# Optimization experiments

Measured on AMD Instinct MI355X. Metric: run time of the kernel, lower is better.

The kernel has to match this reference:

```python
import jax, jax.numpy as jnp
import numpy as np

USR_NUM = 100000
D_IN = 32
D_HID = 32
D_MID = 16
D_OUT = 2
N_EDGES = 1600000
EPS = 1e-16  # matches torch_geometric.utils.softmax denominator eps


def _glorot(key, shape):
    fan_in, fan_out = shape[0], shape[1]
    lim = np.sqrt(6.0 / (fan_in + fan_out))
    return jax.random.uniform(key, shape, jnp.float32, -lim, lim)


def setup_inputs() -> dict:
    key = jax.random.key(0)
    ks = jax.random.split(key, 16)
    inp = {
        "edge_index": jax.random.randint(ks[0], (2, N_EDGES), 0, USR_NUM, dtype=jnp.int64)
        if jax.config.jax_enable_x64 else jax.random.randint(ks[0], (2, N_EDGES), 0, USR_NUM).astype(jnp.int32),
        "emb": jax.random.normal(ks[1], (USR_NUM, D_IN), jnp.float32),
        # conv1: TransformerConv(32 -> 32, heads=1)
        "Wq1": _glorot(ks[2], (D_IN, D_HID)), "bq1": jnp.zeros((D_HID,), jnp.float32),
        "Wk1": _glorot(ks[3], (D_IN, D_HID)), "bk1": jnp.zeros((D_HID,), jnp.float32),
        "Wv1": _glorot(ks[4], (D_IN, D_HID)), "bv1": jnp.zeros((D_HID,), jnp.float32),
        "Ws1": _glorot(ks[5], (D_IN, D_HID)), "bs1": jnp.zeros((D_HID,), jnp.float32),
        # conv2: TransformerConv(32 -> 16, heads=1)
        "Wq2": _glorot(ks[6], (D_HID, D_MID)), "bq2": jnp.zeros((D_MID,), jnp.float32),
        "Wk2": _glorot(ks[7], (D_HID, D_MID)), "bk2": jnp.zeros((D_MID,), jnp.float32),
        "Wv2": _glorot(ks[8], (D_HID, D_MID)), "bv2": jnp.zeros((D_MID,), jnp.float32),
        "Ws2": _glorot(ks[9], (D_HID, D_MID)), "bs2": jnp.zeros((D_MID,), jnp.float32),
        # output: Linear(16 -> 2)
        "Wo": _glorot(ks[10], (D_MID, D_OUT)), "bo": jnp.zeros((D_OUT,), jnp.float32),
    }
    return inp


def transformer_conv(x, src, dst, Wq, bq, Wk, bk, Wv, bv, Ws, bs, n_nodes):
    # edge (j=src -> i=dst): alpha_ij = softmax_i( <q_i, k_j> / sqrt(d) )
    d = Wq.shape[1]
    q = (x @ Wq + bq)[dst]          # [E, d]
    k = (x @ Wk + bk)[src]          # [E, d]
    v = (x @ Wv + bv)[src]          # [E, d]
    alpha = jnp.sum(q * k, axis=-1) / jnp.sqrt(jnp.float32(d))  # [E]
    # segment softmax over incoming edges of each destination node
    seg_max = jax.ops.segment_max(alpha, dst, num_segments=n_nodes)  # [N]
    e = jnp.exp(alpha - seg_max[dst])
    seg_sum = jax.ops.segment_sum(e, dst, num_segments=n_nodes)      # [N]
    w = e / (seg_sum[dst] + EPS)
    agg = jax.ops.segment_sum(v * w[:, None], dst, num_segments=n_nodes)  # [N, d]
    return agg + x @ Ws + bs  # root/skip connection (PyG default root_weight=True)


def reference(edge_index, emb,
              Wq1, bq1, Wk1, bk1, Wv1, bv1, Ws1, bs1,
              Wq2, bq2, Wk2, bk2, Wv2, bv2, Ws2, bs2,
              Wo, bo):
    src, dst = edge_index[0], edge_index[1]
    h = transformer_conv(emb, src, dst, Wq1, bq1, Wk1, bk1, Wv1, bv1, Ws1, bs1, USR_NUM)
    h = jax.nn.relu(h)
    h = transformer_conv(h, src, dst, Wq2, bq2, Wk2, bk2, Wv2, bv2, Ws2, bs2, USR_NUM)
    h = jax.nn.relu(h)
    return h @ Wo + bo  # [N, 2]
```

## Files before the change

kernel.cpp:

```cpp
#include <hip/hip_runtime.h>
#include <hip/hip_bf16.h>

typedef __hip_bfloat16 bf16;
typedef unsigned int uint;
typedef unsigned short ushort;

#define N_NODES 100000
#define N_EDGES_C 1600000
#define NSB 196
#define NSBP 200
#define SBCAP 10240
#define RND 2048
#define EPB (RND / 256)
#define NBIN 64
#define G_RAD ((N_EDGES_C + RND - 1) / RND)
#define NSLOT (NSB * 512)

__device__ __forceinline__ float ldf(const void* p, long i, int isbf) {
    return isbf ? __bfloat162float(((const bf16*)p)[i]) : ((const float*)p)[i];
}
__device__ __forceinline__ int ldidx(const int* ei, long pos, int is64) {
    return is64 ? ei[2 * pos] : ei[pos];
}
__device__ __forceinline__ ushort bfb(float x) {
    bf16 h = __float2bfloat16(x);
    return *(ushort*)&h;
}
__device__ __forceinline__ float bl(uint u) { return __uint_as_float(u << 16); }
__device__ __forceinline__ float bh(uint u) { return __uint_as_float(u & 0xFFFF0000u); }

__global__ void setup_kernel(
    const void* emb, const int* ei,
    const void* Wq1, const void* bq1, const void* Wk1, const void* bk1,
    const void* Wv1, const void* bv1, const void* Ws1, const void* bs1,
    const void* Wq2, const void* bq2, const void* Wk2, const void* bk2,
    const void* Wv2, const void* bv2, const void* Ws2, const void* bs2,
    const void* Wo, const void* bo,
    int* flags, float* wp1, float* bp1, float* wp2, float* bp2, float* woF,
    int* curSB) {
    __shared__ int sf0;
    int t = threadIdx.x;
    if (t < 64) {
        const bf16* pb = (const bf16*)emb;
        int bad = 0;
        for (int i = t; i < 256; i += 64) {
            float v = __bfloat162float(pb[i]);
            if (!(v > -1.0e6f && v < 1.0e6f)) bad++;
        }
        int nz = 0;
        for (int i = 2 * t + 1; i < 256; i += 128) nz += (ei[i] != 0) ? 1 : 0;
#pragma unroll
        for (int m = 32; m >= 1; m >>= 1) {
            bad += __shfl_xor(bad, m, 64);
            nz  += __shfl_xor(nz, m, 64);
        }
        if (t == 0) {
            int f0 = (bad <= 8) ? 1 : 0;
            flags[0] = f0;
            flags[1] = (nz == 0) ? 1 : 0;
            sf0 = f0;
        }
    }
    __syncthreads();
    int isbf = sf0;
    for (int i = t; i < 1024; i += 256) {
        wp1[i]        = ldf(Wq1, i, isbf);
        wp1[1024 + i] = ldf(Wk1, i, isbf);
        wp1[2048 + i] = ldf(Wv1, i, isbf);
        wp1[3072 + i] = ldf(Ws1, i, isbf);
    }
    for (int i = t; i < 512; i += 256) {
        wp2[i]        = ldf(Wq2, i, isbf);
        wp2[512 + i]  = ldf(Wk2, i, isbf);
        wp2[1024 + i] = ldf(Wv2, i, isbf);
        wp2[1536 + i] = ldf(Ws2, i, isbf);
    }
    if (t < 32) {
        bp1[t] = ldf(bq1, t, isbf); bp1[32 + t] = ldf(bk1, t, isbf);
        bp1[64 + t] = ldf(bv1, t, isbf); bp1[96 + t] = ldf(bs1, t, isbf);
        woF[t] = ldf(Wo, t, isbf);
    }
    if (t < 16) {
        bp2[t] = ldf(bq2, t, isbf); bp2[16 + t] = ldf(bk2, t, isbf);
        bp2[32 + t] = ldf(bv2, t, isbf); bp2[48 + t] = ldf(bs2, t, isbf);
    }
    if (t < 2) woF[32 + t] = ldf(bo, t, isbf);
    curSB[t] = 0;
}

template <int DOUT, bool RUNTIME_DTYPE>
__device__ __forceinline__ void node_linear_body(
    const void* __restrict__ X, const float* __restrict__ wpack,
    const float* __restrict__ bpack, const int* __restrict__ flags,
    float* __restrict__ q, ushort* __restrict__ kvb, float* __restrict__ s,
    int bid, float* __restrict__ sW, float* __restrict__ sbias, float* __restrict__ sX) {
    const int TPN = DOUT / 4;
    const int NPB = 256 / TPN;
    const int W_ELEMS = 4 * 32 * DOUT;

    const float4* wp4 = (const float4*)wpack;
    float4* sW4 = (float4*)sW;
    for (int i = threadIdx.x; i < W_ELEMS / 4; i += 256) sW4[i] = wp4[i];
    if (threadIdx.x < 4 * DOUT) sbias[threadIdx.x] = bpack[threadIdx.x];
    const int base = bid * NPB * 32;
    bool useBf = RUNTIME_DTYPE && (flags[0] != 0);
    if (useBf) {
        for (int i = threadIdx.x; i < NPB * 32; i += 256) {
            int g = base + i;
            float xv = (g < N_NODES * 32) ? __bfloat162float(((const bf16*)X)[g]) : 0.0f;
            sX[(i >> 5) * 36 + (i & 31)] = xv;
        }
    } else {
        for (int i = threadIdx.x; i < NPB * 32; i += 256) {
            int g = base + i;
            sX[(i >> 5) * 36 + (i & 31)] = (g < N_NODES * 32) ? ((const float*)X)[g] : 0.0f;
        }
    }
    __syncthreads();

    int l = threadIdx.x / TPN;
    int c4 = (threadIdx.x % TPN) * 4;
    int n = bid * NPB + l;
    if (n >= N_NODES) return;

    float xr[32];
#pragma unroll
    for (int j = 0; j < 8; j++) {
        float4 t4 = *(const float4*)&sX[l * 36 + 4 * j];
        xr[4 * j] = t4.x; xr[4 * j + 1] = t4.y; xr[4 * j + 2] = t4.z; xr[4 * j + 3] = t4.w;
    }
    float acc[4][4];
#pragma unroll
    for (int m = 0; m < 4; m++)
#pragma unroll
        for (int j = 0; j < 4; j++) acc[m][j] = sbias[m * DOUT + c4 + j];

#pragma unroll
    for (int t = 0; t < 32; t++) {
#pragma unroll
        for (int m = 0; m < 4; m++) {
            float4 w = *(const float4*)&sW[(m * 32 + t) * DOUT + c4];
            acc[m][0] += xr[t] * w.x;
            acc[m][1] += xr[t] * w.y;
            acc[m][2] += xr[t] * w.z;
            acc[m][3] += xr[t] * w.w;
        }
    }
    size_t o = (size_t)n * DOUT + c4;
    *(float4*)&q[o] = make_float4(acc[0][0], acc[0][1], acc[0][2], acc[0][3]);
    *(float4*)&s[o] = make_float4(acc[3][0], acc[3][1], acc[3][2], acc[3][3]);
    size_t okv = (size_t)n * 2 * DOUT + c4;
    ushort4 kp = make_ushort4(bfb(acc[1][0]), bfb(acc[1][1]), bfb(acc[1][2]), bfb(acc[1][3]));
    ushort4 vp = make_ushort4(bfb(acc[2][0]), bfb(acc[2][1]), bfb(acc[2][2]), bfb(acc[2][3]));
    *(ushort4*)&kvb[okv]        = kp;
    *(ushort4*)&kvb[okv + DOUT] = vp;
}

struct RadixS {
    int cnt[256]; int excl[256]; int gbase[NSBP];
    uint sVal[RND]; unsigned char sSb[RND];
};
struct LinS { float sW[4096]; float sbias[128]; float sX[32 * 36]; };
union alignas(16) FusedS { RadixS r; LinS l; };

__global__ void fused_ra_nl(
    const int* __restrict__ ei, const int* __restrict__ flags,
    int* __restrict__ curSB, uint* __restrict__ pairsSB,
    const void* __restrict__ X, const float* __restrict__ wpack,
    const float* __restrict__ bpack,
    float* __restrict__ q, ushort* __restrict__ kvb, float* __restrict__ s) {
    __shared__ FusedS u;
    if (blockIdx.x >= G_RAD) {
        node_linear_body<32, true>(X, wpack, bpack, flags, q, kvb, s,
                                   (int)blockIdx.x - G_RAD, u.l.sW, u.l.sbias, u.l.sX);
        return;
    }
    int* cnt = u.r.cnt; int* excl = u.r.excl; int* gbase = u.r.gbase;
    uint* sVal = u.r.sVal; unsigned char* sSb = u.r.sSb;
    const int is64 = flags[1];
    int t = threadIdx.x;
    cnt[t] = 0;
    __syncthreads();
    long base = (long)blockIdx.x * RND;

    int mySb[EPB]; int myRank[EPB]; uint myPk[EPB];
#pragma unroll
    for (int r = 0; r < EPB; r++) {
        long e = base + r * 256 + t;
        mySb[r] = -1;
        if (e < N_EDGES_C) {
            int d = ldidx(ei, (long)N_EDGES_C + e, is64);
            int src = ldidx(ei, e, is64);
            int sb = d >> 9;
            myPk[r] = (uint)src | ((uint)(d & 511) << 17);
            myRank[r] = atomicAdd(&cnt[sb], 1);
            mySb[r] = sb;
        }
    }
    __syncthreads();
    int v = cnt[t];
    excl[t] = v;
    __syncthreads();
    for (int off = 1; off < 256; off <<= 1) {
        int u2 = (t >= off) ? excl[t - off] : 0;
        __syncthreads();
        excl[t] += u2;
        __syncthreads();
    }
    int myExcl = excl[t] - v;
    __syncthreads();
    excl[t] = myExcl;
    __syncthreads();
#pragma unroll
    for (int r = 0; r < EPB; r++) {
        if (mySb[r] >= 0) {
            int pos = excl[mySb[r]] + myRank[r];
            sVal[pos] = myPk[r];
            sSb[pos] = (unsigned char)mySb[r];
        }
    }
    __syncthreads();
    if (t < NSBP)
        gbase[t] = (cnt[t] > 0) ? atomicAdd(&curSB[t], cnt[t]) : 0;
    __syncthreads();
    int tot = excl[NSBP - 1] + cnt[NSBP - 1];
    for (int i = t; i < tot; i += 256) {
        int sb = sSb[i];
        int gp = gbase[sb] + (i - excl[sb]);
        if (gp < SBCAP)
            pairsSB[(size_t)sb * SBCAP + gp] = sVal[i];
    }
}

__global__ void radix_b(const int* __restrict__ curSB, const uint* __restrict__ pairsSB,
                        int* __restrict__ esrc,
                        int* __restrict__ rowbeg, int* __restrict__ rowend,
                        int* __restrict__ perm) {
    __shared__ uint sP[SBCAP];
    __shared__ int dcnt[512], dexcl[512], dcur[512];
    __shared__ int hbin[NBIN], hbase[NBIN], hcur[NBIN];
    int sb = blockIdx.x;
    int t = threadIdx.x;
    int n = min(curSB[sb], SBCAP);
    dcnt[t] = 0; dcur[t] = 0;
    if (t < NBIN) { hbin[t] = 0; hcur[t] = 0; }
    perm[sb * 512 + t] = -1;
    __syncthreads();
    for (int i = t; i < n; i += 512) {
        uint pk = pairsSB[(size_t)sb * SBCAP + i];
        sP[i] = pk;
        atomicAdd(&dcnt[(pk >> 17) & 511], 1);
    }
    __syncthreads();
    int v = dcnt[t];
    dexcl[t] = v;
    __syncthreads();
    for (int off = 1; off < 512; off <<= 1) {
        int u2 = (t >= off) ? dexcl[t - off] : 0;
        __syncthreads();
        dexcl[t] += u2;
        __syncthreads();
    }
    int myExcl = dexcl[t] - v;
    __syncthreads();
    dexcl[t] = myExcl;
    __syncthreads();
    const int EB = sb * SBCAP;
    int dst = sb * 512 + t;
    int mybin = -1;
    if (dst < N_NODES) {
        rowbeg[dst] = EB + myExcl;
        rowend[dst] = EB + myExcl + v;
        mybin = min(v, NBIN - 1);
        atomicAdd(&hbin[mybin], 1);
    }
    __syncthreads();
    if (t < 64) {
        int hv = hbin[t];
        int sfx = hv;
#pragma unroll
        for (int off = 1; off < 64; off <<= 1) {
            int u2 = __shfl_down(sfx, off, 64);
            if (t + off < 64) sfx += u2;
        }
        hbase[t] = sfx - hv;
    }
    __syncthreads();
    if (dst < N_NODES) {
        int r = atomicAdd(&hcur[mybin], 1);
        perm[sb * 512 + hbase[mybin] + r] = dst;
    }
    for (int i = t; i < n; i += 512) {
        uint pk = sP[i];
        int j = (pk >> 17) & 511;
        int p2 = dexcl[j] + atomicAdd(&dcur[j], 1);
        esrc[EB + p2] = (int)(pk & 0x1FFFF);
    }
}

template <int D, bool LAYER2>
__global__ void gather_attn(const int* __restrict__ perm,
                            const int* __restrict__ rowbeg, const int* __restrict__ rowend,
                            const int* __restrict__ esrc,
                            const float* __restrict__ q, const ushort* __restrict__ kvb,
                            const float* __restrict__ s,
                            const float* __restrict__ wp2,
                            const float* __restrict__ bp2,
                            const float* __restrict__ woF,
                            const int* __restrict__ flags,
                            float* __restrict__ q2o, ushort* __restrict__ kvb2o,
                            float* __restrict__ s2o,
                            void* __restrict__ out) {
    const int LPD = D / 8;
    const int G = 64 / LPD;
    __shared__ float sW2[2048];
    __shared__ float sb2[64];
    __shared__ float sH[64 * 36];
    __shared__ int sDst[64];

    if constexpr (!LAYER2) {
        for (int i = threadIdx.x; i < 2048; i += 256) sW2[i] = wp2[i];
        if (threadIdx.x < 64) sb2[threadIdx.x] = bp2[threadIdx.x];
    }

    int lane = threadIdx.x & 63;
    int wave = (blockIdx.x * blockDim.x + threadIdx.x) >> 6;
    int g = lane / LPD;
    int c = lane % LPD;
    int idx = wave * G + g;
    if constexpr (LAYER2) {
        if (idx >= NSLOT) return;
    }
    int dst = perm[idx];
    if constexpr (LAYER2) {
        if (dst < 0) return;
    }
    bool alive = (dst >= 0);

    const float rsq = (D == 32) ? 0.17677669529663689f : 0.25f;
    float4 qa = make_float4(0.f, 0.f, 0.f, 0.f), qb = qa;
    int beg = 0, end = 0;
    if (alive) {
        qa = *(const float4*)(q + (size_t)dst * D + 8 * c);
        qb = *(const float4*)(q + (size_t)dst * D + 8 * c + 4);
        beg = rowbeg[dst]; end = rowend[dst];
    }

    const char* kvbase = (const char*)kvb;
    const int ROW = 4 * D;
    const int koff = 16 * c;
    const int voff = 2 * D + 16 * c;

    float sum0 = 0.f, sum1 = 0.f;
    float a0[8] = {0,0,0,0,0,0,0,0};
    float a1[8] = {0,0,0,0,0,0,0,0};

    uint4 kq[4], vq[4];
#pragma unroll
    for (int r = 0; r < 4; r++) {
        int sn = (beg + r < end) ? esrc[beg + r] : 0;
        const char* p = kvbase + (size_t)sn * ROW;
        kq[r] = *(const uint4*)(p + koff);
        vq[r] = *(const uint4*)(p + voff);
    }

    for (int e = beg; e < end; e += 4) {
        uint4 kc[4], vc[4];
#pragma unroll
        for (int r = 0; r < 4; r++) { kc[r] = kq[r]; vc[r] = vq[r]; }
#pragma unroll
        for (int r = 0; r < 4; r++) {
            if (e + 4 + r < end) {
                const char* p = kvbase + (size_t)esrc[e + 4 + r] * ROW;
                kq[r] = *(const uint4*)(p + koff);
                vq[r] = *(const uint4*)(p + voff);
            }
        }
#pragma unroll
        for (int r = 0; r < 4; r++) {
            if (e + r < end) {
                uint4 kA = kc[r], vA = vc[r];
                float pd = qa.x * bl(kA.x) + qa.y * bh(kA.x) + qa.z * bl(kA.y) + qa.w * bh(kA.y)
                         + qb.x * bl(kA.z) + qb.y * bh(kA.z) + qb.z * bl(kA.w) + qb.w * bh(kA.w);
#pragma unroll
                for (int m = LPD / 2; m >= 1; m >>= 1) pd += __shfl_xor(pd, m, LPD);
                float ex = __expf(fminf(fmaxf(pd * rsq, -80.0f), 80.0f));
                if (r & 1) {
                    sum1 += ex;
                    a1[0] += bl(vA.x) * ex; a1[1] += bh(vA.x) * ex;
                    a1[2] += bl(vA.y) * ex; a1[3] += bh(vA.y) * ex;
                    a1[4] += bl(vA.z) * ex; a1[5] += bh(vA.z) * ex;
                    a1[6] += bl(vA.w) * ex; a1[7] += bh(vA.w) * ex;
                } else {
                    sum0 += ex;
                    a0[0] += bl(vA.x) * ex; a0[1] += bh(vA.x) * ex;
                    a0[2] += bl(vA.y) * ex; a0[3] += bh(vA.y) * ex;
                    a0[4] += bl(vA.z) * ex; a0[5] += bh(vA.z) * ex;
                    a0[6] += bl(vA.w) * ex; a0[7] += bh(vA.w) * ex;
                }
            }
        }
    }
    float inv = 1.0f / (sum0 + sum1 + 1e-16f);
    float4 sa = make_float4(0.f, 0.f, 0.f, 0.f), sbv = sa;
    if (alive) {
        sa  = *(const float4*)(s + (size_t)dst * D + 8 * c);
        sbv = *(const float4*)(s + (size_t)dst * D + 8 * c + 4);
    }
    float h[8];
    h[0] = (a0[0] + a1[0]) * inv + sa.x;  h[1] = (a0[1] + a1[1]) * inv + sa.y;
    h[2] = (a0[2] + a1[2]) * inv + sa.z;  h[3] = (a0[3] + a1[3]) * inv + sa.w;
    h[4] = (a0[4] + a1[4]) * inv + sbv.x; h[5] = (a0[5] + a1[5]) * inv + sbv.y;
    h[6] = (a0[6] + a1[6]) * inv + sbv.z; h[7] = (a0[7] + a1[7]) * inv + sbv.w;
#pragma unroll
    for (int j = 0; j < 8; j++) h[j] = h[j] > 0.0f ? h[j] : 0.0f;

    if constexpr (!LAYER2) {
        int gl = (threadIdx.x >> 6) * G + g;
        if (alive) {
            *(float4*)&sH[gl * 36 + 8 * c]     = make_float4(h[0], h[1], h[2], h[3]);
            *(float4*)&sH[gl * 36 + 8 * c + 4] = make_float4(h[4], h[5], h[6], h[7]);
        }
        if (c == 0) sDst[gl] = dst;
        __syncthreads();
        int l = threadIdx.x >> 2;
        int c4 = (threadIdx.x & 3) * 4;
        int nd = sDst[l];
        if (nd >= 0) {
            float acc2[4][4];
#pragma unroll
            for (int m = 0; m < 4; m++)
#pragma unroll
                for (int j = 0; j < 4; j++) acc2[m][j] = sb2[m * 16 + c4 + j];
#pragma unroll
            for (int t2 = 0; t2 < 32; t2++) {
                float xv = sH[l * 36 + t2];
#pragma unroll
                for (int m = 0; m < 4; m++) {
                    float4 w = *(const float4*)&sW2[(m * 32 + t2) * 16 + c4];
                    acc2[m][0] += xv * w.x;
                    acc2[m][1] += xv * w.y;
                    acc2[m][2] += xv * w.z;
                    acc2[m][3] += xv * w.w;
                }
            }
            size_t o = (size_t)nd * 16 + c4;
            *(float4*)&q2o[o] = make_float4(acc2[0][0], acc2[0][1], acc2[0][2], acc2[0][3]);
            *(float4*)&s2o[o] = make_float4(acc2[3][0], acc2[3][1], acc2[3][2], acc2[3][3]);
            size_t okv = (size_t)nd * 32 + c4;
            ushort4 kp = make_ushort4(bfb(acc2[1][0]), bfb(acc2[1][1]), bfb(acc2[1][2]), bfb(acc2[1][3]));
            ushort4 vp = make_ushort4(bfb(acc2[2][0]), bfb(acc2[2][1]), bfb(acc2[2][2]), bfb(acc2[2][3]));
            *(ushort4*)&kvb2o[okv]      = kp;
            *(ushort4*)&kvb2o[okv + 16] = vp;
        }
    } else {
        float p0 = 0.f, p1 = 0.f;
#pragma unroll
        for (int j = 0; j < 8; j++) {
            p0 += h[j] * woF[(8 * c + j) * 2 + 0];
            p1 += h[j] * woF[(8 * c + j) * 2 + 1];
        }
#pragma unroll
        for (int m = LPD / 2; m >= 1; m >>= 1) {
            p0 += __shfl_xor(p0, m, LPD);
            p1 += __shfl_xor(p1, m, LPD);
        }
        if (c == 0) {
            float o0 = p0 + woF[32];
            float o1 = p1 + woF[33];
            if (flags[0]) {
                ((bf16*)out)[dst * 2 + 0] = __float2bfloat16(o0);
                ((bf16*)out)[dst * 2 + 1] = __float2bfloat16(o1);
            } else {
                ((float*)out)[dst * 2 + 0] = o0;
                ((float*)out)[dst * 2 + 1] = o1;
            }
        }
    }
}

extern "C" void kernel_launch(void* const* d_in, const int* in_sizes, int n_in,
                              void* d_out, int out_size, void* d_ws, size_t ws_size,
                              hipStream_t stream) {
    const int* ei  = (const int*)d_in[0];
    const void* emb = d_in[1];
    const void *Wq1 = d_in[2],  *bq1 = d_in[3];
    const void *Wk1 = d_in[4],  *bk1 = d_in[5];
    const void *Wv1 = d_in[6],  *bv1 = d_in[7];
    const void *Ws1 = d_in[8],  *bs1 = d_in[9];
    const void *Wq2 = d_in[10], *bq2 = d_in[11];
    const void *Wk2 = d_in[12], *bk2 = d_in[13];
    const void *Wv2 = d_in[14], *bv2 = d_in[15];
    const void *Ws2 = d_in[16], *bs2 = d_in[17];
    const void *Wo  = d_in[18], *bo  = d_in[19];

    const size_t ND   = (size_t)N_NODES * 32;
    const size_t ND16 = (size_t)N_NODES * 16;
    const size_t SBTOT = (size_t)NSB * SBCAP;
    float* base   = (float*)d_ws;
    int*   flags  = (int*)base;
    float* wp1    = base + 64;
    float* bp1    = wp1 + 4096;
    float* wp2    = bp1 + 128;
    float* bp2    = wp2 + 2048;
    float* woF    = bp2 + 64;
    int*   curSB  = (int*)(woF + 64);
    int*   rowbeg = curSB + 256;
    int*   rowend = rowbeg + N_NODES;
    int*   perm   = rowend + N_NODES;
    float* p      = (float*)(perm + NSLOT);
    float* q      = p; p += ND;
    float* s      = p; p += ND;
    ushort* kvb   = (ushort*)p; p += ND;
    float* q2     = p; p += ND16;
    float* s2     = p; p += ND16;
    ushort* kvb2  = (ushort*)p; p += ND16;
    int*   esrc   = (int*)p; p += SBTOT;
    uint*  pairsSB = (uint*)p;

    const int B = 256;
    const int gNL32  = (N_NODES + 31) / 32;
    const int gFused = G_RAD + gNL32;
    const int gG1    = NSLOT / 64;
    const int gG2    = NSLOT / 128;

    setup_kernel<<<1, B, 0, stream>>>(emb, ei,
        Wq1, bq1, Wk1, bk1, Wv1, bv1, Ws1, bs1,
        Wq2, bq2, Wk2, bk2, Wv2, bv2, Ws2, bs2, Wo, bo,
        flags, wp1, bp1, wp2, bp2, woF, curSB);

    fused_ra_nl<<<gFused, B, 0, stream>>>(ei, flags, curSB, pairsSB,
                                          emb, wp1, bp1, q, kvb, s);

    radix_b<<<NSB, 512, 0, stream>>>(curSB, pairsSB, esrc, rowbeg, rowend, perm);

    gather_attn<32, false><<<gG1, B, 0, stream>>>(
        perm, rowbeg, rowend, esrc, q, kvb, s, wp2, bp2, nullptr, flags,
        q2, kvb2, s2, nullptr);

    gather_attn<16, true><<<gG2, B, 0, stream>>>(
        perm, rowbeg, rowend, esrc, q2, kvb2, s2, nullptr, nullptr, woF, flags,
        nullptr, nullptr, nullptr, d_out);
}
```

Before: 265.8 us.

## Split radix second pass into half-superbucket blocks and deepen gather prefetch

Measured after the change: 289.9 us. +9.1%, slower.

```diff
diff --git a/kernel.cpp b/kernel.cpp
--- a/kernel.cpp
+++ b/kernel.cpp
@@ -14,7 +14,9 @@
 #define EPB (RND / 256)
 #define NBIN 64
 #define G_RAD ((N_EDGES_C + RND - 1) / RND)
-#define NSLOT (NSB * 512)
+#define NHB 392
+#define HCAP 5632
+#define NSLOT (NHB * 256)
 
 __device__ __forceinline__ float ldf(const void* p, long i, int isbf) {
     return isbf ? __bfloat162float(((const bf16*)p)[i]) : ((const float*)p)[i];
@@ -163,7 +165,7 @@
 struct LinS { float sW[4096]; float sbias[128]; float sX[32 * 36]; };
 union alignas(16) FusedS { RadixS r; LinS l; };
 
-__global__ void fused_ra_nl(
+__global__ void __launch_bounds__(256, 4) fused_ra_nl(
     const int* __restrict__ ei, const int* __restrict__ flags,
     int* __restrict__ curSB, uint* __restrict__ pairsSB,
     const void* __restrict__ X, const float* __restrict__ wpack,
@@ -232,30 +234,39 @@
     }
 }
 
-__global__ void radix_b(const int* __restrict__ curSB, const uint* __restrict__ pairsSB,
-                        int* __restrict__ esrc,
-                        int* __restrict__ rowbeg, int* __restrict__ rowend,
-                        int* __restrict__ perm) {
-    __shared__ uint sP[SBCAP];
-    __shared__ int dcnt[512], dexcl[512], dcur[512];
+__global__ void __launch_bounds__(256, 4) radix_b(
+    const int* __restrict__ curSB, const uint* __restrict__ pairsSB,
+    int* __restrict__ esrc,
+    int* __restrict__ rowbeg, int* __restrict__ rowend,
+    int* __restrict__ perm) {
+    __shared__ uint sP[HCAP];
+    __shared__ int dcnt[256], dexcl[256], dcur[256];
     __shared__ int hbin[NBIN], hbase[NBIN], hcur[NBIN];
-    int sb = blockIdx.x;
+    __shared__ int scnt;
+    int sbh = blockIdx.x;
+    int parent = sbh >> 1, half = sbh & 1;
     int t = threadIdx.x;
-    int n = min(curSB[sb], SBCAP);
+    int n = min(curSB[parent], SBCAP);
     dcnt[t] = 0; dcur[t] = 0;
     if (t < NBIN) { hbin[t] = 0; hcur[t] = 0; }
-    perm[sb * 512 + t] = -1;
-    __syncthreads();
-    for (int i = t; i < n; i += 512) {
-        uint pk = pairsSB[(size_t)sb * SBCAP + i];
-        sP[i] = pk;
-        atomicAdd(&dcnt[(pk >> 17) & 511], 1);
-    }
-    __syncthreads();
+    if (t == 0) scnt = 0;
+    perm[sbh * 256 + t] = -1;
+    __syncthreads();
+    const uint* srcp = pairsSB + (size_t)parent * SBCAP;
+    for (int i = t; i < n; i += 256) {
+        uint pk = srcp[i];
+        if (((pk >> 25) & 1u) == (uint)half) {
+            int m = atomicAdd(&scnt, 1);
+            if (m < HCAP) sP[m] = pk;
+            atomicAdd(&dcnt[(pk >> 17) & 255], 1);
+        }
+    }
+    __syncthreads();
+    int nc = min(scnt, HCAP);
     int v = dcnt[t];
     dexcl[t] = v;
     __syncthreads();
-    for (int off = 1; off < 512; off <<= 1) {
+    for (int off = 1; off < 256; off <<= 1) {
         int u2 = (t >= off) ? dexcl[t - off] : 0;
         __syncthreads();
         dexcl[t] += u2;
@@ -265,12 +276,14 @@
     __syncthreads();
     dexcl[t] = myExcl;
     __syncthreads();
-    const int EB = sb * SBCAP;
-    int dst = sb * 512 + t;
+    const int EB = sbh * HCAP;
+    int dst = sbh * 256 + t;
     int mybin = -1;
     if (dst < N_NODES) {
-        rowbeg[dst] = EB + myExcl;
-        rowend[dst] = EB + myExcl + v;
+        int rb = min(myExcl, HCAP);
+        int re = min(myExcl + v, HCAP);
+        rowbeg[dst] = EB + rb;
+        rowend[dst] = EB + re;
         mybin = min(v, NBIN - 1);
         atomicAdd(&hbin[mybin], 1);
     }
@@ -288,18 +301,19 @@
     __syncthreads();
     if (dst < N_NODES) {
         int r = atomicAdd(&hcur[mybin], 1);
-        perm[sb * 512 + hbase[mybin] + r] = dst;
-    }
-    for (int i = t; i < n; i += 512) {
+        perm[sbh * 256 + hbase[mybin] + r] = dst;
+    }
+    for (int i = t; i < nc; i += 256) {
         uint pk = sP[i];
-        int j = (pk >> 17) & 511;
+        int j = (pk >> 17) & 255;
         int p2 = dexcl[j] + atomicAdd(&dcur[j], 1);
-        esrc[EB + p2] = (int)(pk & 0x1FFFF);
+        if (p2 < HCAP) esrc[EB + p2] = (int)(pk & 0x1FFFF);
     }
 }
 
 template <int D, bool LAYER2>
-__global__ void gather_attn(const int* __restrict__ perm,
+__global__ void __launch_bounds__(256, 2) gather_attn(
+                            const int* __restrict__ perm,
                             const int* __restrict__ rowbeg, const int* __restrict__ rowend,
                             const int* __restrict__ esrc,
                             const float* __restrict__ q, const ushort* __restrict__ kvb,
@@ -355,29 +369,37 @@
     float a0[8] = {0,0,0,0,0,0,0,0};
     float a1[8] = {0,0,0,0,0,0,0,0};
 
-    uint4 kq[4], vq[4];
-#pragma unroll
-    for (int r = 0; r < 4; r++) {
+    uint4 kq[8], vq[8];
+    int sn1[8];
+#pragma unroll
+    for (int r = 0; r < 8; r++) {
         int sn = (beg + r < end) ? esrc[beg + r] : 0;
         const char* p = kvbase + (size_t)sn * ROW;
         kq[r] = *(const uint4*)(p + koff);
         vq[r] = *(const uint4*)(p + voff);
     }
-
-    for (int e = beg; e < end; e += 4) {
-        uint4 kc[4], vc[4];
-#pragma unroll
-        for (int r = 0; r < 4; r++) { kc[r] = kq[r]; vc[r] = vq[r]; }
-#pragma unroll
-        for (int r = 0; r < 4; r++) {
-            if (e + 4 + r < end) {
-                const char* p = kvbase + (size_t)esrc[e + 4 + r] * ROW;
+#pragma unroll
+    for (int r = 0; r < 8; r++)
+        sn1[r] = (beg + 8 + r < end) ? esrc[beg + 8 + r] : 0;
+
+    for (int e = beg; e < end; e += 8) {
+        uint4 kc[8], vc[8];
+#pragma unroll
+        for (int r = 0; r < 8; r++) { kc[r] = kq[r]; vc[r] = vq[r]; }
+#pragma unroll
+        for (int r = 0; r < 8; r++) {
+            if (e + 8 + r < end) {
+                const char* p = kvbase + (size_t)sn1[r] * ROW;
                 kq[r] = *(const uint4*)(p + koff);
                 vq[r] = *(const uint4*)(p + voff);
             }
         }
 #pragma unroll
-        for (int r = 0; r < 4; r++) {
+        for (int r = 0; r < 8; r++) {
+            if (e + 16 + r < end) sn1[r] = esrc[e + 16 + r];
+        }
+#pragma unroll
+        for (int r = 0; r < 8; r++) {
             if (e + r < end) {
                 uint4 kA = kc[r], vA = vc[r];
                 float pd = qa.x * bl(kA.x) + qa.y * bh(kA.x) + qa.z * bl(kA.y) + qa.w * bh(kA.y)
@@ -497,6 +519,7 @@
     const size_t ND   = (size_t)N_NODES * 32;
     const size_t ND16 = (size_t)N_NODES * 16;
     const size_t SBTOT = (size_t)NSB * SBCAP;
+    const size_t ESRC_TOT = (size_t)NHB * HCAP;
     float* base   = (float*)d_ws;
     int*   flags  = (int*)base;
     float* wp1    = base + 64;
@@ -515,7 +538,7 @@
     float* q2     = p; p += ND16;
     float* s2     = p; p += ND16;
     ushort* kvb2  = (ushort*)p; p += ND16;
-    int*   esrc   = (int*)p; p += SBTOT;
+    int*   esrc   = (int*)p; p += ESRC_TOT;
     uint*  pairsSB = (uint*)p;
 
     const int B = 256;
@@ -532,7 +555,7 @@
     fused_ra_nl<<<gFused, B, 0, stream>>>(ei, flags, curSB, pairsSB,
                                           emb, wp1, bp1, q, kvb, s);
 
-    radix_b<<<NSB, 512, 0, stream>>>(curSB, pairsSB, esrc, rowbeg, rowend, perm);
+    radix_b<<<NHB, B, 0, stream>>>(curSB, pairsSB, esrc, rowbeg, rowend, perm);
 
     gather_attn<32, false><<<gG1, B, 0, stream>>>(
         perm, rowbeg, rowend, esrc, q, kvb, s, wp2, bp2, nullptr, flags,
```
